# Kernel tuning notes

Hardware: AMD Instinct MI355X
Metric: run time of the kernel (lower is better)

## Reference

```python
import jax, jax.numpy as jnp
import numpy as np

N, D, E_EDGES = 50000, 128, 800000
HEADS, REL_DIM, N_RELS, LAYERS = 4, 64, 64, 2
HD = HEADS * D  # per-head out_channels == d_model (concat=False)
LN_EPS = 1e-5
NEG_SLOPE = 0.2


def setup_inputs() -> dict:
    key = jax.random.key(0)
    ks = jax.random.split(key, 12)
    s = 0.02
    return {
        "x_flat": jax.random.normal(ks[0], (N, D), jnp.float32),
        "edge_index": jax.random.randint(ks[1], (2, E_EDGES), 0, N, jnp.int32),
        "edge_type": jax.random.randint(ks[2], (E_EDGES,), 0, N_RELS, jnp.int32),
        "rel_emb": jax.random.normal(ks[3], (N_RELS, REL_DIM), jnp.float32) * s,
        # stacked params for LAYERS GATv2Conv layers
        "Wl": jax.random.normal(ks[4], (LAYERS, D, HD), jnp.float32) * s,
        "bl": jnp.zeros((LAYERS, HD), jnp.float32),
        "Wr": jax.random.normal(ks[5], (LAYERS, D, HD), jnp.float32) * s,
        "br": jnp.zeros((LAYERS, HD), jnp.float32),
        "We": jax.random.normal(ks[6], (LAYERS, REL_DIM, HD), jnp.float32) * s,
        "att": jax.random.normal(ks[7], (LAYERS, HEADS, D), jnp.float32) * s,
        "b_out": jnp.zeros((LAYERS, D), jnp.float32),
        "ln_g": jnp.ones((LAYERS, D), jnp.float32),
        "ln_b": jnp.zeros((LAYERS, D), jnp.float32),
    }


def _gatv2_layer(h, src, dst, eattr, Wl, bl, Wr, br, We, att, b_out):
    # h: [N, D] -> per-head transforms [N, H, C]
    xl = (h @ Wl + bl).reshape(N, HEADS, D)   # source transform (messages)
    xr = (h @ Wr + br).reshape(N, HEADS, D)   # target transform
    xe = (eattr @ We).reshape(-1, HEADS, D)   # edge transform (no bias, PyG)
    # GATv2 attention: a^T leaky_relu(xl_j + xr_i + xe)
    s = jax.nn.leaky_relu(xl[src] + xr[dst] + xe, NEG_SLOPE)  # [E, H, C]
    logits = jnp.einsum('ehc,hc->eh', s, att)                  # [E, H]
    # segment softmax over destination nodes
    mx = jax.ops.segment_max(logits, dst, num_segments=N)      # [N, H]
    ex = jnp.exp(logits - mx[dst])
    den = jax.ops.segment_sum(ex, dst, num_segments=N)
    alpha = ex / den[dst]                                      # [E, H]
    msg = xl[src] * alpha[..., None]                           # [E, H, C]
    out = jax.ops.segment_sum(msg.reshape(-1, HD), dst, num_segments=N)
    out = out.reshape(N, HEADS, D).mean(axis=1) + b_out        # concat=False -> mean
    return out


def _layernorm(x, g, b):
    mu = x.mean(-1, keepdims=True)
    var = ((x - mu) ** 2).mean(-1, keepdims=True)
    return (x - mu) * jax.lax.rsqrt(var + LN_EPS) * g + b


def reference(x_flat, edge_index, edge_type, rel_emb, Wl, bl, Wr, br, We, att, b_out, ln_g, ln_b):
    src, dst = edge_index[0], edge_index[1]
    eattr = rel_emb[edge_type]  # [E, REL_DIM]
    h = x_flat
    for l in range(LAYERS):
        m = _gatv2_layer(h, src, dst, eattr, Wl[l], bl[l], Wr[l], br[l], We[l], att[l], b_out[l])
        m = jax.nn.gelu(m, approximate=False)  # dropout in eval mode
        h = _layernorm(h + m, ln_g[l], ln_b[l])
    return h
```

## Files before the change

kernel.cpp:

```cpp
#include <hip/hip_runtime.h>
#include <hip/hip_bf16.h>

#define NN 50000
#define DM 128
#define EE 800000
#define NH 4
#define HDIM 512
#define NRELS 64
#define RDIM 64
#define LAYERS 2
#define NB 196

#define PM_HB 6250
#define PM_WC 1024
#define PM_XE 256
#define PM_CZ 196
#define PM_TOT (PM_HB + PM_WC + PM_XE + PM_CZ + 1)

typedef short frag8 __attribute__((ext_vector_type(8)));
typedef float f32x4 __attribute__((ext_vector_type(4)));
typedef float f32x2 __attribute__((ext_vector_type(2)));

__device__ __forceinline__ float b2f(unsigned short u) {
    unsigned v = ((unsigned)u) << 16;
    union { unsigned u; float f; } c; c.u = v; return c.f;
}
__device__ __forceinline__ float b2f_lo(unsigned u) {
    union { unsigned u; float f; } c; c.u = u << 16; return c.f;
}
__device__ __forceinline__ float b2f_hi(unsigned u) {
    union { unsigned u; float f; } c; c.u = u & 0xFFFF0000u; return c.f;
}
__device__ __forceinline__ unsigned short f2b(float f) {
    union { float f; unsigned u; } c; c.f = f;
    unsigned u = c.u;
    u += 0x7FFFu + ((u >> 16) & 1u);
    return (unsigned short)(u >> 16);
}

template<int CTRL>
__device__ __forceinline__ float dpp_add(float x) {
    int yi = __builtin_amdgcn_update_dpp(0, __builtin_bit_cast(int, x),
                                         CTRL, 0xF, 0xF, true);
    return x + __builtin_bit_cast(float, yi);
}

__global__ void count_kernel(const int* __restrict__ dst, int* __restrict__ counts) {
    int e = blockIdx.x * 256 + threadIdx.x;
    if (e < EE) atomicAdd(&counts[dst[e]], 1);
}

__global__ __launch_bounds__(256) void psum_kernel(const int* __restrict__ counts,
                                                   int* __restrict__ psums) {
    int idx = blockIdx.x * 256 + threadIdx.x;
    int x = (idx < NN) ? counts[idx] : 0;
    int lane = threadIdx.x & 63, wv = threadIdx.x >> 6;
    #pragma unroll
    for (int d = 1; d < 64; d <<= 1) x += __shfl_xor(x, d, 64);
    __shared__ int ws[4];
    if (lane == 0) ws[wv] = x;
    __syncthreads();
    if (threadIdx.x == 0) psums[blockIdx.x] = ws[0] + ws[1] + ws[2] + ws[3];
}

__global__ __launch_bounds__(256) void pscan_kernel(const int* __restrict__ psums,
                                                    int* __restrict__ offs,
                                                    int* __restrict__ row_ptr) {
    int t = threadIdx.x;
    int x = (t < NB) ? psums[t] : 0;
    int lane = t & 63, wv = t >> 6;
    int incl = x;
    #pragma unroll
    for (int d = 1; d < 64; d <<= 1) {
        int y = __shfl_up(incl, d, 64);
        if (lane >= d) incl += y;
    }
    __shared__ int ws[4];
    if (lane == 63) ws[wv] = incl;
    __syncthreads();
    int off = 0;
    for (int k = 0; k < wv; ++k) off += ws[k];
    if (t < NB) offs[t] = incl + off - x;
    if (t == 0) row_ptr[0] = 0;
}

__global__ __launch_bounds__(256) void pfin_kernel(const int* __restrict__ counts,
                                                   const int* __restrict__ offs,
                                                   int* __restrict__ row_ptr,
                                                   int* __restrict__ cursor) {
    int idx = blockIdx.x * 256 + threadIdx.x;
    int x = (idx < NN) ? counts[idx] : 0;
    int lane = threadIdx.x & 63, wv = threadIdx.x >> 6;
    int incl = x;
    #pragma unroll
    for (int d = 1; d < 64; d <<= 1) {
        int y = __shfl_up(incl, d, 64);
        if (lane >= d) incl += y;
    }
    __shared__ int ws[4];
    if (lane == 63) ws[wv] = incl;
    __syncthreads();
    int off = offs[blockIdx.x];
    for (int k = 0; k < wv; ++k) off += ws[k];
    if (idx < NN) {
        int v = off + incl;
        row_ptr[idx + 1] = v;
        cursor[idx] = v - x;
    }
}

__global__ void scatter_pk_kernel(const int* __restrict__ ei, const int* __restrict__ etype,
                                  int* __restrict__ cursor, unsigned* __restrict__ pkq) {
    int e = blockIdx.x * 256 + threadIdx.x;
    if (e < EE) {
        int d = ei[EE + e];
        int p = atomicAdd(&cursor[d], 1);
        pkq[p] = ((unsigned)ei[e] << 6) | (unsigned)etype[e];
    }
}

__global__ __launch_bounds__(256) void prep_misc_kernel(
    const float* __restrict__ x_flat,
    const float* __restrict__ Wl, const float* __restrict__ Wr,
    const float* __restrict__ rel_emb, const float* __restrict__ We,
    const float* __restrict__ att,
    unsigned short* __restrict__ hb, unsigned short* __restrict__ Wt,
    unsigned short* __restrict__ xeb, float* __restrict__ be,
    int* __restrict__ counts) {
    int b = blockIdx.x, t = threadIdx.x;
    if (b < PM_HB) {
        int idx = b * 256 + t;
        float4 v = ((const float4*)x_flat)[idx];
        ushort4 o;
        o.x = f2b(v.x); o.y = f2b(v.y); o.z = f2b(v.z); o.w = f2b(v.w);
        ((ushort4*)hb)[idx] = o;
        return;
    }
    b -= PM_HB;
    if (b < PM_WC) {
        int idx = b * 256 + t;
        int m = idx >> 16;
        int r = idx & 65535;
        int c = r >> 7, k = r & 127;
        int l = m >> 1;
        const float* W = (m & 1) ? Wr : Wl;
        Wt[idx] = f2b(W[(size_t)l * DM * HDIM + k * HDIM + c]);
        return;
    }
    b -= PM_WC;
    if (b < PM_XE) {
        int idx = b * 256 + t;
        int l  = idx / (NRELS * HDIM);
        int r  = (idx / HDIM) & (NRELS - 1);
        int hc = idx & (HDIM - 1);
        const float* Wel = We + (size_t)l * RDIM * HDIM;
        float s = 0.f;
        #pragma unroll 8
        for (int d = 0; d < RDIM; ++d) s += rel_emb[r * RDIM + d] * Wel[d * HDIM + hc];
        xeb[idx] = f2b(s);
        return;
    }
    b -= PM_XE;
    if (b < PM_CZ) {
        int idx = b * 256 + t;
        if (idx < NN) counts[idx] = 0;
        return;
    }
    __shared__ float aw_s[LAYERS * NH * RDIM];
    #pragma unroll
    for (int k = 0; k < 2; ++k) {
        int idx = t * 2 + k;
        int l = idx >> 8, h = (idx >> 6) & 3, d = idx & 63;
        const float* ap = att + (size_t)l * HDIM + h * DM;
        const float* wp = We + (size_t)l * RDIM * HDIM + (size_t)d * HDIM + h * DM;
        float s = 0.f;
        #pragma unroll 8
        for (int c = 0; c < DM; ++c) s += ap[c] * wp[c];
        aw_s[idx] = s;
    }
    __syncthreads();
    #pragma unroll
    for (int k = 0; k < 2; ++k) {
        int idx = t * 2 + k;
        int l = idx >> 8, r = (idx >> 2) & 63, h = idx & 3;
        const float* rp = rel_emb + r * RDIM;
        const float* ap = aw_s + l * 256 + h * 64;
        float s = 0.f;
        #pragma unroll 8
        for (int d = 0; d < RDIM; ++d) s += rp[d] * ap[d];
        be[idx] = 0.6f * s;
    }
}

__global__ __launch_bounds__(256) void gemm_xlxr_ab_kernel(
    const unsigned short* __restrict__ hb,
    const unsigned short* __restrict__ WtL,
    const unsigned short* __restrict__ WtR,
    const float* __restrict__ bl, const float* __restrict__ br,
    const float* __restrict__ att_l,
    unsigned short* __restrict__ xl, unsigned short* __restrict__ xr,
    float* __restrict__ ab) {
    int w = threadIdx.x >> 6, lane = threadIdx.x & 63;
    int m0 = blockIdx.x * 32;
    int colL = lane & 15, kg = lane >> 4;

    frag8 a[2][4];
    #pragma unroll
    for (int mt = 0; mt < 2; ++mt) {
        int row = m0 + mt * 16 + colL;
        if (row >= NN) row = NN - 1;
        const unsigned short* arow = hb + (size_t)row * DM;
        #pragma unroll
        for (int kc = 0; kc < 4; ++kc) {
            uint4 raw = *(const uint4*)(arow + kc * 32 + kg * 8);
            a[mt][kc] = __builtin_bit_cast(frag8, raw);
        }
    }

    float prow[2][2][4];
    #pragma unroll
    for (int mt = 0; mt < 2; ++mt)
        #pragma unroll
        for (int mat = 0; mat < 2; ++mat)
            #pragma unroll
            for (int r = 0; r < 4; ++r) prow[mt][mat][r] = 0.f;

    #pragma unroll
    for (int mat = 0; mat < 2; ++mat) {
        const unsigned short* Wt = mat ? WtR : WtL;
        const float* bias = mat ? br : bl;
        unsigned short* out = mat ? xr : xl;
        #pragma unroll
        for (int nt = 0; nt < 8; ++nt) {
            int col = w * 128 + nt * 16 + colL;
            f32x4 acc0 = {0.f, 0.f, 0.f, 0.f};
            f32x4 acc1 = {0.f, 0.f, 0.f, 0.f};
            #pragma unroll
            for (int kc = 0; kc < 4; ++kc) {
                uint4 raw = *(const uint4*)(Wt + (size_t)col * DM + kc * 32 + kg * 8);
                frag8 b = __builtin_bit_cast(frag8, raw);
                acc0 = __builtin_amdgcn_mfma_f32_16x16x32_bf16(a[0][kc], b, acc0, 0, 0, 0);
                acc1 = __builtin_amdgcn_mfma_f32_16x16x32_bf16(a[1][kc], b, acc1, 0, 0, 0);
            }
            float bb = bias[col];
            float ac = att_l[col];
            #pragma unroll
            for (int r = 0; r < 4; ++r) {
                float v0 = acc0[r] + bb;
                float v1 = acc1[r] + bb;
                int row0 = m0 + kg * 4 + r;
                int row1 = row0 + 16;
                if (row0 < NN) out[(size_t)row0 * HDIM + col] = f2b(v0);
                if (row1 < NN) out[(size_t)row1 * HDIM + col] = f2b(v1);
                prow[0][mat][r] = fmaf(ac, v0, prow[0][mat][r]);
                prow[1][mat][r] = fmaf(ac, v1, prow[1][mat][r]);
            }
        }
    }
    #pragma unroll
    for (int d = 1; d < 16; d <<= 1) {
        #pragma unroll
        for (int mt = 0; mt < 2; ++mt)
            #pragma unroll
            for (int mat = 0; mat < 2; ++mat)
                #pragma unroll
                for (int r = 0; r < 4; ++r)
                    prow[mt][mat][r] += __shfl_xor(prow[mt][mat][r], d, 64);
    }
    if (colL == 0) {
        #pragma unroll
        for (int mt = 0; mt < 2; ++mt) {
            int row = m0 + mt * 16 + kg * 4;
            #pragma unroll
            for (int mat = 0; mat < 2; ++mat)
                #pragma unroll
                for (int r = 0; r < 4; ++r)
                    if (row + r < NN)
                        ab[(size_t)(row + r) * 8 + mat * 4 + w] = 0.6f * prow[mt][mat][r];
        }
    }
}

__global__ __launch_bounds__(256) void node_fused_kernel(
    const int* __restrict__ row_ptr,
    const unsigned* __restrict__ pkq,
    const unsigned short* __restrict__ xl,
    const unsigned short* __restrict__ xr,
    const unsigned short* __restrict__ xeb_l,
    const float* __restrict__ ab,
    const float* __restrict__ be_l,
    const float* __restrict__ att_l,
    const float* __restrict__ h_in,
    const float* __restrict__ b_out, const float* __restrict__ ln_g,
    const float* __restrict__ ln_b,
    float* __restrict__ h_out,
    unsigned short* __restrict__ hb_out) {
    int w = threadIdx.x >> 6, l = threadIdx.x & 63;
    int i = blockIdx.x * 4 + w;
    int hh = l >> 4;
    __shared__ float cl[4][64][4];
    __shared__ unsigned pk_s[4][64];

    int beg = row_ptr[i], end = row_ptr[i + 1];
    int c0 = (l & 15) * 8;

    uint4 xrv = *(const uint4*)(xr + (size_t)i * HDIM + l * 8);
    f32x2 xrp0 = f32x2{b2f_lo(xrv.x), b2f_hi(xrv.x)};
    f32x2 xrp1 = f32x2{b2f_lo(xrv.y), b2f_hi(xrv.y)};
    f32x2 xrp2 = f32x2{b2f_lo(xrv.z), b2f_hi(xrv.z)};
    f32x2 xrp3 = f32x2{b2f_lo(xrv.w), b2f_hi(xrv.w)};
    float4 at0 = ((const float4*)(att_l + l * 8))[0];
    float4 at1 = ((const float4*)(att_l + l * 8))[1];
    float atv[8] = {at0.x * 0.4f, at0.y * 0.4f, at0.z * 0.4f, at0.w * 0.4f,
                    at1.x * 0.4f, at1.y * 0.4f, at1.z * 0.4f, at1.w * 0.4f};
    float4 bxv = ((const float4*)ab)[2 * i + 1];
    float4 hv0 = *(const float4*)(h_in + (size_t)i * DM + c0);
    float4 hv1 = *(const float4*)(h_in + (size_t)i * DM + c0 + 4);

    const char* xl_b = (const char*)xl;
    const char* xe_b = (const char*)xeb_l;
    uint l16 = (uint)l << 4;

    float ss = 0.f;
    f32x2 acc0 = f32x2{0.f, 0.f}, acc1 = f32x2{0.f, 0.f};
    f32x2 acc2 = f32x2{0.f, 0.f}, acc3 = f32x2{0.f, 0.f};

    for (int cb = beg; cb < end; cb += 64) {
        int mc = min(64, end - cb);
        if (l < mc) {
            unsigned pk = pkq[cb + l];
            pk_s[w][l] = pk;
            int s = pk >> 6, r = pk & 63;
            float4 a4 = ((const float4*)ab)[2 * s];
            float4 b4 = ((const float4*)be_l)[r];
            cl[w][l][0] = a4.x + b4.x + bxv.x;
            cl[w][l][1] = a4.y + b4.y + bxv.y;
            cl[w][l][2] = a4.z + b4.z + bxv.z;
            cl[w][l][3] = a4.w + b4.w + bxv.w;
        }
        unsigned pk0 = pk_s[w][0];
        uint4 vvP = *(const uint4*)(xl_b + ((pk0 >> 6) << 10) + l16);
        uint4 eeP = *(const uint4*)(xe_b + ((pk0 & 63u) << 10) + l16);
        float cjP = cl[w][0][hh];
        for (int j = 1; j <= mc; ++j) {
            uint4 vv = vvP; uint4 ee = eeP; float cj = cjP;
            if (j < mc) {
                unsigned pkj = pk_s[w][j];
                vvP = *(const uint4*)(xl_b + ((pkj >> 6) << 10) + l16);
                eeP = *(const uint4*)(xe_b + ((pkj & 63u) << 10) + l16);
                cjP = cl[w][j][hh];
            }
            f32x2 xp0 = f32x2{b2f_lo(vv.x), b2f_hi(vv.x)};
            f32x2 xp1 = f32x2{b2f_lo(vv.y), b2f_hi(vv.y)};
            f32x2 xp2 = f32x2{b2f_lo(vv.z), b2f_hi(vv.z)};
            f32x2 xp3 = f32x2{b2f_lo(vv.w), b2f_hi(vv.w)};
            f32x2 z0 = (xp0 + xrp0) + f32x2{b2f_lo(ee.x), b2f_hi(ee.x)};
            f32x2 z1 = (xp1 + xrp1) + f32x2{b2f_lo(ee.y), b2f_hi(ee.y)};
            f32x2 z2 = (xp2 + xrp2) + f32x2{b2f_lo(ee.z), b2f_hi(ee.z)};
            f32x2 z3 = (xp3 + xrp3) + f32x2{b2f_lo(ee.w), b2f_hi(ee.w)};
            float partial = fmaf(atv[0], fabsf(z0[0]),
                            fmaf(atv[1], fabsf(z0[1]),
                            fmaf(atv[2], fabsf(z1[0]),
                            fmaf(atv[3], fabsf(z1[1]),
                            fmaf(atv[4], fabsf(z2[0]),
                            fmaf(atv[5], fabsf(z2[1]),
                            fmaf(atv[6], fabsf(z3[0]), atv[7] * fabsf(z3[1]))))))));
            partial = dpp_add<0xB1>(partial);
            partial = dpp_add<0x4E>(partial);
            partial = dpp_add<0x124>(partial);
            partial = dpp_add<0x128>(partial);
            float we = __expf(partial + cj);
            ss += we;
            f32x2 wv = f32x2{we, we};
            acc0 += wv * xp0;
            acc1 += wv * xp1;
            acc2 += wv * xp2;
            acc3 += wv * xp3;
        }
    }

    float invs = (ss > 0.f) ? 1.f / ss : 0.f;
    float sv[8] = {acc0[0] * invs, acc0[1] * invs, acc1[0] * invs, acc1[1] * invs,
                   acc2[0] * invs, acc2[1] * invs, acc3[0] * invs, acc3[1] * invs};
    #pragma unroll
    for (int d = 16; d < 64; d <<= 1)
        #pragma unroll
        for (int k = 0; k < 8; ++k) sv[k] += __shfl_xor(sv[k], d, 64);

    float4 bo0 = *(const float4*)(b_out + c0);
    float4 bo1 = *(const float4*)(b_out + c0 + 4);
    float bov[8] = {bo0.x, bo0.y, bo0.z, bo0.w, bo1.x, bo1.y, bo1.z, bo1.w};
    float hvv[8] = {hv0.x, hv0.y, hv0.z, hv0.w, hv1.x, hv1.y, hv1.z, hv1.w};
    float yv[8];
    float la = 0.f, lb = 0.f;
    #pragma unroll
    for (int k = 0; k < 8; ++k) {
        float o = sv[k] * 0.25f + bov[k];
        float ge = 0.5f * o * (1.f + erff(o * 0.70710678118654752f));
        float y = hvv[k] + ge;
        yv[k] = y; la += y; lb += y * y;
    }
    la = dpp_add<0xB1>(la); la = dpp_add<0x4E>(la);
    la = dpp_add<0x124>(la); la = dpp_add<0x128>(la);
    lb = dpp_add<0xB1>(lb); lb = dpp_add<0x4E>(lb);
    lb = dpp_add<0x124>(lb); lb = dpp_add<0x128>(lb);
    float mean = la * (1.f / 128.f);
    float var = lb * (1.f / 128.f) - mean * mean;
    float rs = rsqrtf(var + 1e-5f);

    if (l < 16) {
        float4 g0 = *(const float4*)(ln_g + c0);
        float4 g1 = *(const float4*)(ln_g + c0 + 4);
        float4 q0 = *(const float4*)(ln_b + c0);
        float4 q1 = *(const float4*)(ln_b + c0 + 4);
        float gv[8] = {g0.x, g0.y, g0.z, g0.w, g1.x, g1.y, g1.z, g1.w};
        float qv[8] = {q0.x, q0.y, q0.z, q0.w, q1.x, q1.y, q1.z, q1.w};
        float ov[8];
        #pragma unroll
        for (int k = 0; k < 8; ++k)
            ov[k] = (yv[k] - mean) * rs * gv[k] + qv[k];
        float* hop = h_out + (size_t)i * DM + c0;
        *(float4*)hop = make_float4(ov[0], ov[1], ov[2], ov[3]);
        *(float4*)(hop + 4) = make_float4(ov[4], ov[5], ov[6], ov[7]);
        uint4 ob;
        ob.x = (unsigned)f2b(ov[0]) | ((unsigned)f2b(ov[1]) << 16);
        ob.y = (unsigned)f2b(ov[2]) | ((unsigned)f2b(ov[3]) << 16);
        ob.z = (unsigned)f2b(ov[4]) | ((unsigned)f2b(ov[5]) << 16);
        ob.w = (unsigned)f2b(ov[6]) | ((unsigned)f2b(ov[7]) << 16);
        *(uint4*)(hb_out + (size_t)i * DM + c0) = ob;
    }
}

extern "C" void kernel_launch(void* const* d_in, const int* in_sizes, int n_in,
                              void* d_out, int out_size, void* d_ws, size_t ws_size,
                              hipStream_t stream) {
    const float* x_flat   = (const float*)d_in[0];
    const int*   edge_idx = (const int*)d_in[1];
    const int*   edge_ty  = (const int*)d_in[2];
    const float* rel_emb  = (const float*)d_in[3];
    const float* Wl       = (const float*)d_in[4];
    const float* bl       = (const float*)d_in[5];
    const float* Wr       = (const float*)d_in[6];
    const float* br       = (const float*)d_in[7];
    const float* We       = (const float*)d_in[8];
    const float* att      = (const float*)d_in[9];
    const float* b_out    = (const float*)d_in[10];
    const float* ln_g     = (const float*)d_in[11];
    const float* ln_b     = (const float*)d_in[12];

    char* p = (char*)d_ws;
    auto carve = [&](size_t bytes) {
        void* r = (void*)p;
        p += (bytes + 255) & ~(size_t)255;
        return r;
    };
    unsigned short* xl     = (unsigned short*)carve((size_t)NN * HDIM * 2);
    unsigned short* xr     = (unsigned short*)carve((size_t)NN * HDIM * 2);
    float*          h1     = (float*)carve((size_t)NN * DM * 4);
    unsigned short* hb     = (unsigned short*)carve((size_t)NN * DM * 2);
    unsigned short* Wt     = (unsigned short*)carve((size_t)4 * DM * HDIM * 2);
    unsigned short* xeb    = (unsigned short*)carve((size_t)LAYERS * NRELS * HDIM * 2);
    float*          ab     = (float*)carve((size_t)NN * 8 * 4);
    float*          be     = (float*)carve((size_t)LAYERS * NRELS * NH * 4);
    int*            row_ptr= (int*)carve((size_t)(NN + 1) * 4);
    int*            counts = (int*)carve((size_t)NN * 4);
    int*            cursor = (int*)carve((size_t)NN * 4);
    int*            psums  = (int*)carve((size_t)NB * 4);
    int*            offs   = (int*)carve((size_t)NB * 4);
    unsigned*       pkq    = (unsigned*)carve((size_t)EE * 4);

    const int* dst = edge_idx + EE;

    prep_misc_kernel<<<PM_TOT, 256, 0, stream>>>(
        x_flat, Wl, Wr, rel_emb, We, att, hb, Wt, xeb, be, counts);

    count_kernel<<<(EE + 255) / 256, 256, 0, stream>>>(dst, counts);
    psum_kernel<<<NB, 256, 0, stream>>>(counts, psums);
    pscan_kernel<<<1, 256, 0, stream>>>(psums, offs, row_ptr);
    pfin_kernel<<<NB, 256, 0, stream>>>(counts, offs, row_ptr, cursor);
    scatter_pk_kernel<<<(EE + 255) / 256, 256, 0, stream>>>(edge_idx, edge_ty, cursor, pkq);

    const float* h_cur = x_flat;
    for (int l = 0; l < LAYERS; ++l) {
        float* h_next = (l == LAYERS - 1) ? (float*)d_out : h1;
        gemm_xlxr_ab_kernel<<<(NN + 31) / 32, 256, 0, stream>>>(
            hb,
            Wt + (size_t)(l * 2 + 0) * DM * HDIM,
            Wt + (size_t)(l * 2 + 1) * DM * HDIM,
            bl + (size_t)l * HDIM, br + (size_t)l * HDIM,
            att + (size_t)l * HDIM,
            xl, xr, ab);
        node_fused_kernel<<<NN / 4, 256, 0, stream>>>(
            row_ptr, pkq, xl, xr,
            xeb + (size_t)l * NRELS * HDIM,
            ab, be + (size_t)l * NRELS * NH,
            att + (size_t)l * HDIM,
            h_cur,
            b_out + (size_t)l * DM, ln_g + (size_t)l * DM, ln_b + (size_t)l * DM,
            h_next, hb);
        h_cur = h_next;
    }
}
```

Before: 558.3 us.

## Enlarge GEMM row tile to 64, pre-shift edge offsets, skip bf16 hi masking

The xl/xr projection GEMM now gives each block 64 rows instead of 32, so every loaded weight fragment feeds four MFMAs rather than two. The cost is more accumulator and A-fragment registers per thread. The packed edge record grows from 4 to 8 bytes and stores the source and relation indices already shifted by 10, which removes the per-edge shift and mask in the node gather loop. The high-half bf16 unpack also drops its mask and uses the raw 32-bit word, accepting a tiny error from the low bits in exchange for one fewer ALU op per element.

```diff
diff --git a/kernel.cpp b/kernel.cpp
--- a/kernel.cpp
+++ b/kernel.cpp
@@ -31,6 +31,9 @@
 __device__ __forceinline__ float b2f_hi(unsigned u) {
     union { unsigned u; float f; } c; c.u = u & 0xFFFF0000u; return c.f;
 }
+__device__ __forceinline__ float b2f_hi_raw(unsigned u) {
+    union { unsigned u; float f; } c; c.u = u; return c.f;
+}
 __device__ __forceinline__ unsigned short f2b(float f) {
     union { float f; unsigned u; } c; c.f = f;
     unsigned u = c.u;
@@ -110,12 +113,15 @@
 }
 
 __global__ void scatter_pk_kernel(const int* __restrict__ ei, const int* __restrict__ etype,
-                                  int* __restrict__ cursor, unsigned* __restrict__ pkq) {
+                                  int* __restrict__ cursor, uint2* __restrict__ pkq) {
     int e = blockIdx.x * 256 + threadIdx.x;
     if (e < EE) {
         int d = ei[EE + e];
         int p = atomicAdd(&cursor[d], 1);
-        pkq[p] = ((unsigned)ei[e] << 6) | (unsigned)etype[e];
+        uint2 v;
+        v.x = (unsigned)ei[e] << 10;
+        v.y = (unsigned)etype[e] << 10;
+        pkq[p] = v;
     }
 }
 
@@ -201,12 +207,12 @@
     unsigned short* __restrict__ xl, unsigned short* __restrict__ xr,
     float* __restrict__ ab) {
     int w = threadIdx.x >> 6, lane = threadIdx.x & 63;
-    int m0 = blockIdx.x * 32;
+    int m0 = blockIdx.x * 64;
     int colL = lane & 15, kg = lane >> 4;
 
-    frag8 a[2][4];
-    #pragma unroll
-    for (int mt = 0; mt < 2; ++mt) {
+    frag8 a[4][4];
+    #pragma unroll
+    for (int mt = 0; mt < 4; ++mt) {
         int row = m0 + mt * 16 + colL;
         if (row >= NN) row = NN - 1;
         const unsigned short* arow = hb + (size_t)row * DM;
@@ -217,9 +223,9 @@
         }
     }
 
-    float prow[2][2][4];
-    #pragma unroll
-    for (int mt = 0; mt < 2; ++mt)
+    float prow[4][2][4];
+    #pragma unroll
+    for (int mt = 0; mt < 4; ++mt)
         #pragma unroll
         for (int mat = 0; mat < 2; ++mat)
             #pragma unroll
@@ -233,34 +239,35 @@
         #pragma unroll
         for (int nt = 0; nt < 8; ++nt) {
             int col = w * 128 + nt * 16 + colL;
-            f32x4 acc0 = {0.f, 0.f, 0.f, 0.f};
-            f32x4 acc1 = {0.f, 0.f, 0.f, 0.f};
+            f32x4 acc[4];
+            #pragma unroll
+            for (int mt = 0; mt < 4; ++mt) acc[mt] = f32x4{0.f, 0.f, 0.f, 0.f};
             #pragma unroll
             for (int kc = 0; kc < 4; ++kc) {
                 uint4 raw = *(const uint4*)(Wt + (size_t)col * DM + kc * 32 + kg * 8);
                 frag8 b = __builtin_bit_cast(frag8, raw);
-                acc0 = __builtin_amdgcn_mfma_f32_16x16x32_bf16(a[0][kc], b, acc0, 0, 0, 0);
-                acc1 = __builtin_amdgcn_mfma_f32_16x16x32_bf16(a[1][kc], b, acc1, 0, 0, 0);
+                #pragma unroll
+                for (int mt = 0; mt < 4; ++mt)
+                    acc[mt] = __builtin_amdgcn_mfma_f32_16x16x32_bf16(a[mt][kc], b, acc[mt], 0, 0, 0);
             }
             float bb = bias[col];
             float ac = att_l[col];
             #pragma unroll
-            for (int r = 0; r < 4; ++r) {
-                float v0 = acc0[r] + bb;
-                float v1 = acc1[r] + bb;
-                int row0 = m0 + kg * 4 + r;
-                int row1 = row0 + 16;
-                if (row0 < NN) out[(size_t)row0 * HDIM + col] = f2b(v0);
-                if (row1 < NN) out[(size_t)row1 * HDIM + col] = f2b(v1);
-                prow[0][mat][r] = fmaf(ac, v0, prow[0][mat][r]);
-                prow[1][mat][r] = fmaf(ac, v1, prow[1][mat][r]);
+            for (int mt = 0; mt < 4; ++mt) {
+                #pragma unroll
+                for (int r = 0; r < 4; ++r) {
+                    float v = acc[mt][r] + bb;
+                    int row = m0 + mt * 16 + kg * 4 + r;
+                    if (row < NN) out[(size_t)row * HDIM + col] = f2b(v);
+                    prow[mt][mat][r] = fmaf(ac, v, prow[mt][mat][r]);
+                }
             }
         }
     }
     #pragma unroll
     for (int d = 1; d < 16; d <<= 1) {
         #pragma unroll
-        for (int mt = 0; mt < 2; ++mt)
+        for (int mt = 0; mt < 4; ++mt)
             #pragma unroll
             for (int mat = 0; mat < 2; ++mat)
                 #pragma unroll
@@ -269,7 +276,7 @@
     }
     if (colL == 0) {
         #pragma unroll
-        for (int mt = 0; mt < 2; ++mt) {
+        for (int mt = 0; mt < 4; ++mt) {
             int row = m0 + mt * 16 + kg * 4;
             #pragma unroll
             for (int mat = 0; mat < 2; ++mat)
@@ -283,7 +290,7 @@
 
 __global__ __launch_bounds__(256) void node_fused_kernel(
     const int* __restrict__ row_ptr,
-    const unsigned* __restrict__ pkq,
+    const uint2* __restrict__ pkq,
     const unsigned short* __restrict__ xl,
     const unsigned short* __restrict__ xr,
     const unsigned short* __restrict__ xeb_l,
@@ -299,7 +306,7 @@
     int i = blockIdx.x * 4 + w;
     int hh = l >> 4;
     __shared__ float cl[4][64][4];
-    __shared__ unsigned pk_s[4][64];
+    __shared__ uint2 pk_s[4][64];
 
     int beg = row_ptr[i], end = row_ptr[i + 1];
     int c0 = (l & 15) * 8;
@@ -328,9 +335,9 @@
     for (int cb = beg; cb < end; cb += 64) {
         int mc = min(64, end - cb);
         if (l < mc) {
-            unsigned pk = pkq[cb + l];
+            uint2 pk = pkq[cb + l];
             pk_s[w][l] = pk;
-            int s = pk >> 6, r = pk & 63;
+            int s = pk.x >> 10, r = pk.y >> 10;
             float4 a4 = ((const float4*)ab)[2 * s];
             float4 b4 = ((const float4*)be_l)[r];
             cl[w][l][0] = a4.x + b4.x + bxv.x;
@@ -338,26 +345,26 @@
             cl[w][l][2] = a4.z + b4.z + bxv.z;
             cl[w][l][3] = a4.w + b4.w + bxv.w;
         }
-        unsigned pk0 = pk_s[w][0];
-        uint4 vvP = *(const uint4*)(xl_b + ((pk0 >> 6) << 10) + l16);
-        uint4 eeP = *(const uint4*)(xe_b + ((pk0 & 63u) << 10) + l16);
+        uint2 pk0 = pk_s[w][0];
+        uint4 vvP = *(const uint4*)(xl_b + pk0.x + l16);
+        uint4 eeP = *(const uint4*)(xe_b + pk0.y + l16);
         float cjP = cl[w][0][hh];
         for (int j = 1; j <= mc; ++j) {
             uint4 vv = vvP; uint4 ee = eeP; float cj = cjP;
             if (j < mc) {
-                unsigned pkj = pk_s[w][j];
-                vvP = *(const uint4*)(xl_b + ((pkj >> 6) << 10) + l16);
-                eeP = *(const uint4*)(xe_b + ((pkj & 63u) << 10) + l16);
+                uint2 pkj = pk_s[w][j];
+                vvP = *(const uint4*)(xl_b + pkj.x + l16);
+                eeP = *(const uint4*)(xe_b + pkj.y + l16);
                 cjP = cl[w][j][hh];
             }
-            f32x2 xp0 = f32x2{b2f_lo(vv.x), b2f_hi(vv.x)};
-            f32x2 xp1 = f32x2{b2f_lo(vv.y), b2f_hi(vv.y)};
-            f32x2 xp2 = f32x2{b2f_lo(vv.z), b2f_hi(vv.z)};
-            f32x2 xp3 = f32x2{b2f_lo(vv.w), b2f_hi(vv.w)};
-            f32x2 z0 = (xp0 + xrp0) + f32x2{b2f_lo(ee.x), b2f_hi(ee.x)};
-            f32x2 z1 = (xp1 + xrp1) + f32x2{b2f_lo(ee.y), b2f_hi(ee.y)};
-            f32x2 z2 = (xp2 + xrp2) + f32x2{b2f_lo(ee.z), b2f_hi(ee.z)};
-            f32x2 z3 = (xp3 + xrp3) + f32x2{b2f_lo(ee.w), b2f_hi(ee.w)};
+            f32x2 xp0 = f32x2{b2f_lo(vv.x), b2f_hi_raw(vv.x)};
+            f32x2 xp1 = f32x2{b2f_lo(vv.y), b2f_hi_raw(vv.y)};
+            f32x2 xp2 = f32x2{b2f_lo(vv.z), b2f_hi_raw(vv.z)};
+            f32x2 xp3 = f32x2{b2f_lo(vv.w), b2f_hi_raw(vv.w)};
+            f32x2 z0 = (xp0 + xrp0) + f32x2{b2f_lo(ee.x), b2f_hi_raw(ee.x)};
+            f32x2 z1 = (xp1 + xrp1) + f32x2{b2f_lo(ee.y), b2f_hi_raw(ee.y)};
+            f32x2 z2 = (xp2 + xrp2) + f32x2{b2f_lo(ee.z), b2f_hi_raw(ee.z)};
+            f32x2 z3 = (xp3 + xrp3) + f32x2{b2f_lo(ee.w), b2f_hi_raw(ee.w)};
             float partial = fmaf(atv[0], fabsf(z0[0]),
                             fmaf(atv[1], fabsf(z0[1]),
                             fmaf(atv[2], fabsf(z1[0]),
@@ -467,7 +474,7 @@
     int*            cursor = (int*)carve((size_t)NN * 4);
     int*            psums  = (int*)carve((size_t)NB * 4);
     int*            offs   = (int*)carve((size_t)NB * 4);
-    unsigned*       pkq    = (unsigned*)carve((size_t)EE * 4);
+    uint2*          pkq    = (uint2*)carve((size_t)EE * 8);
 
     const int* dst = edge_idx + EE;
 
@@ -483,7 +490,7 @@
     const float* h_cur = x_flat;
     for (int l = 0; l < LAYERS; ++l) {
         float* h_next = (l == LAYERS - 1) ? (float*)d_out : h1;
-        gemm_xlxr_ab_kernel<<<(NN + 31) / 32, 256, 0, stream>>>(
+        gemm_xlxr_ab_kernel<<<(NN + 63) / 64, 256, 0, stream>>>(
             hb,
             Wt + (size_t)(l * 2 + 0) * DM * HDIM,
             Wt + (size_t)(l * 2 + 1) * DM * HDIM,
```

Result: slower. 606.3 us (+8.6%).
